# Performance work log

Measured on AMD Instinct MI355X. Metric: run time of the kernel, lower is better.

The kernel has to match this reference:

```python
import jax, jax.numpy as jnp
import numpy as np

B, S, F = 8, 8192, 11
D_MODEL, D_STATE, D_CONV, EXPAND, N_LAYERS = 128, 16, 4, 2, 4
D_INNER = EXPAND * D_MODEL
DT_RANK = (D_MODEL + 15) // 16  # ceil(d_model/16) = 8


def setup_inputs() -> dict:
    key = jax.random.key(0)
    ks = jax.random.split(key, 12)
    inp = {
        "features": jax.random.normal(ks[0], (B, S, F), jnp.float32),
        "emb_w": jax.random.normal(ks[1], (F, D_MODEL), jnp.float32) * 0.1,
        "emb_b": jnp.zeros((D_MODEL,), jnp.float32),
        "in_proj_w": jax.random.normal(ks[2], (N_LAYERS, D_MODEL, 2 * D_INNER), jnp.float32) * (D_MODEL ** -0.5),
        "conv_w": jax.random.normal(ks[3], (N_LAYERS, D_INNER, D_CONV), jnp.float32) * 0.3,
        "conv_b": jnp.zeros((N_LAYERS, D_INNER), jnp.float32),
        "x_proj_w": jax.random.normal(ks[4], (N_LAYERS, D_INNER, DT_RANK + 2 * D_STATE), jnp.float32) * (D_INNER ** -0.5),
        "dt_w": jax.random.normal(ks[5], (N_LAYERS, DT_RANK, D_INNER), jnp.float32) * (DT_RANK ** -0.5),
        "dt_b": jax.random.normal(ks[6], (N_LAYERS, D_INNER), jnp.float32) * 0.1 - 4.0,  # softplus -> small dt
        # canonical S4D-real init: A_log = log(1..d_state), per channel
        "A_log": jnp.broadcast_to(jnp.log(jnp.arange(1, D_STATE + 1, dtype=jnp.float32)), (N_LAYERS, D_INNER, D_STATE)).copy(),
        "D": jnp.ones((N_LAYERS, D_INNER), jnp.float32),
        "out_proj_w": jax.random.normal(ks[7], (N_LAYERS, D_INNER, D_MODEL), jnp.float32) * (D_INNER ** -0.5),
        "head_w": jax.random.normal(ks[8], (D_MODEL, 1), jnp.float32) * (D_MODEL ** -0.5),
        "head_b": jnp.zeros((1,), jnp.float32),
    }
    return inp


def _mamba_layer(x, in_w, cw, cb, xp_w, dtw, dtb, A_log, Dp, out_w):
    # x: [B,S,d_model]
    xz = x @ in_w                       # [B,S,2*d_inner]
    u, z = jnp.split(xz, 2, axis=-1)    # each [B,S,d_inner]
    # causal depthwise conv1d over sequence
    uc = jnp.transpose(u, (0, 2, 1))    # [B,d_inner,S]
    kern = cw[:, None, :]               # [d_inner,1,d_conv]
    conv = jax.lax.conv_general_dilated(
        uc, kern, window_strides=(1,), padding=[(D_CONV - 1, 0)],
        dimension_numbers=("NCH", "OIH", "NCH"), feature_group_count=D_INNER)
    u = jax.nn.silu(jnp.transpose(conv, (0, 2, 1)) + cb)   # [B,S,d_inner]
    x_dbl = u @ xp_w                                        # [B,S,dt_rank+2N]
    dt, Bm, Cm = jnp.split(x_dbl, [DT_RANK, DT_RANK + D_STATE], axis=-1)
    delta = jax.nn.softplus(dt @ dtw + dtb)                 # [B,S,d_inner]
    A = -jnp.exp(A_log)                                     # [d_inner,N]

    def step(h, inp):
        d_t, b_t, c_t, u_t = inp        # [B,d_inner],[B,N],[B,N],[B,d_inner]
        dA = jnp.exp(d_t[:, :, None] * A)                   # [B,d_inner,N]
        h = h * dA + (d_t * u_t)[:, :, None] * b_t[:, None, :]
        y = jnp.einsum("bdn,bn->bd", h, c_t)
        return h, y

    h0 = jnp.zeros((x.shape[0], D_INNER, D_STATE), x.dtype)
    xs = (jnp.transpose(delta, (1, 0, 2)), jnp.transpose(Bm, (1, 0, 2)),
          jnp.transpose(Cm, (1, 0, 2)), jnp.transpose(u, (1, 0, 2)))
    _, ys = jax.lax.scan(step, h0, xs)                      # ys: [S,B,d_inner]
    y = jnp.transpose(ys, (1, 0, 2)) + u * Dp
    y = y * jax.nn.silu(z)
    return y @ out_w                                        # [B,S,d_model]


def reference(features, emb_w, emb_b, in_proj_w, conv_w, conv_b, x_proj_w,
              dt_w, dt_b, A_log, D, out_proj_w, head_w, head_b):
    x = features @ emb_w + emb_b
    for i in range(N_LAYERS):
        x = _mamba_layer(x, in_proj_w[i], conv_w[i], conv_b[i], x_proj_w[i],
                         dt_w[i], dt_b[i], A_log[i], D[i], out_proj_w[i])
    logits = x @ head_w + head_b
    return jax.nn.sigmoid(logits)       # [B,S,1]
```

## Files before the change

kernel.cpp:

```cpp
#include <hip/hip_runtime.h>

#define BB 8
#define SS 8192
#define FF 11
#define DM 128
#define DSTATE 16
#define DI 256
#define NL 4
#define DTR 8
#define TT (BB*SS)
#define NCHUNK 256
#define LCHUNK (SS/NCHUNK)

typedef __bf16 bf16x8 __attribute__((ext_vector_type(8)));
typedef float f32x4 __attribute__((ext_vector_type(4)));

__device__ __forceinline__ ushort f2bf(float f) {
    union { float f; unsigned u; } v; v.f = f;
    unsigned r = v.u + 0x7FFF + ((v.u >> 16) & 1);
    return (ushort)(r >> 16);
}
__device__ __forceinline__ float b2f(ushort h) {
    union { unsigned u; float f; } v; v.u = ((unsigned)h) << 16;
    return v.f;
}
__device__ __forceinline__ float rcpf(float x) { return __builtin_amdgcn_rcpf(x); }

__device__ __forceinline__ void dA_powers(float e1, float* dA) {
    float p2 = e1 * e1, p4 = p2 * p2, p8 = p4 * p4;
    dA[0] = e1;  dA[1] = p2;       dA[2] = p2 * e1;  dA[3] = p4;
    dA[4] = p4 * e1; dA[5] = p4 * p2; dA[6] = p4 * dA[2]; dA[7] = p8;
#pragma unroll
    for (int i = 8; i < 16; ++i) dA[i] = p8 * dA[i - 8];
}

__device__ __forceinline__ void del_e1(float x, float& del, float& e1) {
    float ex = __expf(x);
    e1 = rcpf(1.f + ex);
    del = (x > 20.f) ? x : -__logf(e1);
}

__global__ void k_prep(const float* __restrict__ inpw, const float* __restrict__ xpw,
                       const float* __restrict__ outw, const float* __restrict__ ew,
                       const float* __restrict__ eb, const float* __restrict__ hw,
                       ushort* __restrict__ WtIn, ushort* __restrict__ WtXp,
                       ushort* __restrict__ WtOut, float* __restrict__ W1,
                       float* __restrict__ wh) {
    int task = blockIdx.y;
    int idx = blockIdx.x * 256 + threadIdx.x;
    if (task < 4) {
        int l = task, tot = 512 * 128;
        if (idx >= tot) return;
        int n = idx >> 7, k = idx & 127;
        float v = inpw[(size_t)l * 128 * 512 + (size_t)k * 512 + n];
        WtIn[(size_t)l * tot + idx] = f2bf(v);
    } else if (task < 8) {
        int l = task - 4, tot = 64 * 256;
        if (idx >= tot) return;
        int n = idx >> 8, k = idx & 255;
        float v = (n < 40) ? xpw[(size_t)l * 256 * 40 + (size_t)k * 40 + n] : 0.f;
        WtXp[(size_t)l * tot + idx] = f2bf(v);
    } else if (task < 12) {
        int l = task - 8, tot = 128 * 256;
        if (idx >= tot) return;
        int n = idx >> 8, k = idx & 255;
        float v = outw[(size_t)l * 256 * 128 + (size_t)k * 128 + n];
        WtOut[(size_t)l * tot + idx] = f2bf(v);
    } else if (task == 12) {
        if (idx >= 12 * 512) return;
        int f = idx >> 9, n = idx & 511;
        const float* src = (f < FF) ? (ew + f * DM) : eb;
        float acc = 0.f;
#pragma unroll 4
        for (int dm = 0; dm < DM; ++dm) acc = fmaf(src[dm], inpw[(size_t)dm * 512 + n], acc);
        W1[idx] = acc;
    } else {
        if (idx >= 256) return;
        float acc = 0.f;
#pragma unroll 4
        for (int dm = 0; dm < DM; ++dm)
            acc = fmaf(outw[(size_t)3 * DI * DM + (size_t)idx * DM + dm], hw[dm], acc);
        wh[idx] = acc;
    }
}

__global__ __launch_bounds__(256) void k_xz0(const float* __restrict__ feat,
                                             const float* __restrict__ W1,
                                             ushort* __restrict__ xz) {
    int tid = threadIdx.x;
    int n0 = (tid & 127) * 4;
    int rsub = tid >> 7;
    int r0 = blockIdx.x * 16 + rsub * 8;
    f32x4 wv[12];
#pragma unroll
    for (int f = 0; f < 12; ++f) wv[f] = *(const f32x4*)&W1[f * 512 + n0];
#pragma unroll
    for (int k = 0; k < 8; ++k) {
        int r = r0 + k;
        const float* fr = feat + (size_t)r * FF;
        f32x4 a = wv[11];
#pragma unroll
        for (int f = 0; f < FF; ++f) a += fr[f] * wv[f];
        ushort4 o;
        o.x = f2bf(a[0]); o.y = f2bf(a[1]); o.z = f2bf(a[2]); o.w = f2bf(a[3]);
        *(ushort4*)&xz[(size_t)r * 512 + n0] = o;
    }
}

template<bool OUT_BF16>
__global__ __launch_bounds__(256) void k_mgemm(const ushort* __restrict__ A,
                                               const ushort* __restrict__ Wt,
                                               void* __restrict__ Cv,
                                               int N, int K) {
    __shared__ __align__(16) ushort As[128 * 64];
    const int tid  = threadIdx.x;
    const int lane = tid & 63, wv = tid >> 6;
    const int m0 = blockIdx.x * 128;
    const int n0 = blockIdx.y * 64;
    const int lrow = lane >> 3;
    const int kcg  = (lane & 7) ^ lrow;
    const int mrow = lane & 15;
    const int kq   = lane >> 4;

    f32x4 acc[2][4];
#pragma unroll
    for (int i = 0; i < 2; ++i)
#pragma unroll
        for (int j = 0; j < 4; ++j) acc[i][j] = (f32x4){0.f, 0.f, 0.f, 0.f};

    const int rl0 = (wv << 5) + mrow;
    const int rl1 = rl0 + 16;
    const ushort* bg[4];
#pragma unroll
    for (int jt = 0; jt < 4; ++jt)
        bg[jt] = Wt + (size_t)(n0 + (jt << 4) + mrow) * K + (kq << 3);

    for (int k0 = 0; k0 < K; k0 += 64) {
        if (k0) __syncthreads();
#pragma unroll
        for (int i = 0; i < 4; ++i) {
            int issue = (wv << 2) + i;
            int row = (issue << 3) + lrow;
            const ushort* gp = A + (size_t)(m0 + row) * K + k0 + (kcg << 3);
            __builtin_amdgcn_global_load_lds(
                (const __attribute__((address_space(1))) void*)gp,
                (__attribute__((address_space(3))) void*)(As + (issue << 9)),
                16, 0, 0);
        }
        __syncthreads();
#pragma unroll
        for (int ks = 0; ks < 2; ++ks) {
            int kqg = (ks << 2) + kq;
            bf16x8 a0 = *(const bf16x8*)&As[(rl0 << 6) + ((kqg ^ (rl0 & 7)) << 3)];
            bf16x8 a1 = *(const bf16x8*)&As[(rl1 << 6) + ((kqg ^ (rl1 & 7)) << 3)];
#pragma unroll
            for (int jt = 0; jt < 4; ++jt) {
                bf16x8 b = *(const bf16x8*)(bg[jt] + k0 + (ks << 5));
                acc[0][jt] = __builtin_amdgcn_mfma_f32_16x16x32_bf16(a0, b, acc[0][jt], 0, 0, 0);
                acc[1][jt] = __builtin_amdgcn_mfma_f32_16x16x32_bf16(a1, b, acc[1][jt], 0, 0, 0);
            }
        }
    }
    int crow = m0 + (wv << 5) + (kq << 2);
    int ccol = n0 + mrow;
#pragma unroll
    for (int i = 0; i < 2; ++i)
#pragma unroll
        for (int jt = 0; jt < 4; ++jt)
#pragma unroll
            for (int rg = 0; rg < 4; ++rg) {
                int row = crow + (i << 4) + rg;
                int col = ccol + (jt << 4);
                if (OUT_BF16) {
                    ((ushort*)Cv)[(size_t)row * N + col] = f2bf(acc[i][jt][rg]);
                } else {
                    if (col < N) ((float*)Cv)[(size_t)row * N + col] = acc[i][jt][rg];
                }
            }
}

__global__ __launch_bounds__(256) void k_convxp(const ushort* __restrict__ xz,
                                                const float* __restrict__ cw,
                                                const float* __restrict__ cb,
                                                const ushort* __restrict__ WtXp_l,
                                                ushort* __restrict__ uc,
                                                float* __restrict__ xdbl) {
    __shared__ __align__(16) ushort us[32 * 256];
    int tid = threadIdx.x;
    int cg = tid & 63;
    int tsub = tid >> 6;
    int r0b = blockIdx.x * 32;
    int r0 = r0b + tsub * 8;
    int d0 = cg * 4;
    int tloc = r0 & (SS - 1);

    float w[4][4], bias[4];
#pragma unroll
    for (int j = 0; j < 4; ++j) {
        bias[j] = cb[d0 + j];
        float4 wj = *(const float4*)&cw[(d0 + j) * 4];
        w[j][0] = wj.x; w[j][1] = wj.y; w[j][2] = wj.z; w[j][3] = wj.w;
    }
    float xv[11][4];
#pragma unroll
    for (int i = 0; i < 11; ++i) {
        ushort4 v = make_ushort4(0, 0, 0, 0);
        if (tloc + i >= 3)
            v = *(const ushort4*)&xz[(size_t)(r0 + i - 3) * 512 + d0];
        xv[i][0] = b2f(v.x); xv[i][1] = b2f(v.y);
        xv[i][2] = b2f(v.z); xv[i][3] = b2f(v.w);
    }
#pragma unroll
    for (int k = 0; k < 8; ++k) {
        float a[4] = {bias[0], bias[1], bias[2], bias[3]};
#pragma unroll
        for (int j = 0; j < 4; ++j)
#pragma unroll
            for (int ch = 0; ch < 4; ++ch)
                a[ch] = fmaf(xv[k + j][ch], w[ch][j], a[ch]);
        ushort4 o;
        o.x = f2bf(a[0] * rcpf(1.f + __expf(-a[0])));
        o.y = f2bf(a[1] * rcpf(1.f + __expf(-a[1])));
        o.z = f2bf(a[2] * rcpf(1.f + __expf(-a[2])));
        o.w = f2bf(a[3] * rcpf(1.f + __expf(-a[3])));
        *(ushort4*)&uc[(size_t)(r0 + k) * DI + d0] = o;
        int lr = tsub * 8 + k;
        int addr = lr * 256 + (((cg >> 1) ^ (lr & 7)) << 3) + ((cg & 1) << 2);
        *(ushort4*)&us[addr] = o;
    }
    __syncthreads();
    int lane = tid & 63, wvi = tid >> 6;
    int mt = wvi & 1;
    int nt0 = (wvi >> 1) * 2;
    int mrow = lane & 15, kq = lane >> 4;
    f32x4 acc0 = (f32x4){0.f, 0.f, 0.f, 0.f};
    f32x4 acc1 = (f32x4){0.f, 0.f, 0.f, 0.f};
    int arow = mt * 16 + mrow;
    const ushort* bg0 = WtXp_l + (size_t)(nt0 * 16 + mrow) * 256 + (kq << 3);
    const ushort* bg1 = bg0 + 16 * 256;
#pragma unroll
    for (int k0 = 0; k0 < 256; k0 += 32) {
        int chunk = (k0 >> 3) + kq;
        bf16x8 a = *(const bf16x8*)&us[arow * 256 + ((chunk ^ (arow & 7)) << 3)];
        bf16x8 b0 = *(const bf16x8*)(bg0 + k0);
        bf16x8 b1 = *(const bf16x8*)(bg1 + k0);
        acc0 = __builtin_amdgcn_mfma_f32_16x16x32_bf16(a, b0, acc0, 0, 0, 0);
        acc1 = __builtin_amdgcn_mfma_f32_16x16x32_bf16(a, b1, acc1, 0, 0, 0);
    }
    int row = r0b + mt * 16 + (kq << 2);
    int col0 = nt0 * 16 + mrow;
    int col1 = col0 + 16;
#pragma unroll
    for (int rg = 0; rg < 4; ++rg) {
        if (col0 < 40) xdbl[(size_t)(row + rg) * 40 + col0] = acc0[rg];
        if (col1 < 40) xdbl[(size_t)(row + rg) * 40 + col1] = acc1[rg];
    }
}

__global__ __launch_bounds__(256) void k_scanA(const float* __restrict__ xdbl,
                                               ushort* __restrict__ uc,
                                               const float* __restrict__ dtw,
                                               const float* __restrict__ dtb,
                                               const float* __restrict__ Dp,
                                               ushort* __restrict__ hloc,
                                               float* __restrict__ sumd) {
    int d = threadIdx.x;
    int c = blockIdx.x & (NCHUNK - 1);
    int b = blockIdx.x >> 8;
    float wdt[8];
#pragma unroll
    for (int j = 0; j < 8; ++j) wdt[j] = dtw[j * DI + d];
    float bdt = dtb[d];
    float Dd = Dp[d];
    float h[16] = {};
    float sd = 0.f;
    size_t rbase = (size_t)(b * SS + c * LCHUNK);
    const float* __restrict__ rwp = xdbl + rbase * 40;
    ushort* __restrict__ up = uc + rbase * DI + d;
    float ut = b2f(up[0]);
    float cur[40];
#pragma unroll
    for (int j = 0; j < 40; ++j) cur[j] = rwp[j];
    for (int tt = 0; tt < LCHUNK; ++tt) {
        float nxt[40];
        const float* rn = rwp + (tt + 1) * 40;
#pragma unroll
        for (int j = 0; j < 40; ++j) nxt[j] = rn[j];
        float utn = b2f(up[(tt + 1) * DI]);
        float x = bdt;
#pragma unroll
        for (int j = 0; j < 8; ++j) x = fmaf(cur[j], wdt[j], x);
        float del, e1;
        del_e1(x, del, e1);
        float du = del * ut;
        float dA[16];
        dA_powers(e1, dA);
        float y = 0.f;
#pragma unroll
        for (int n = 0; n < 16; ++n) {
            h[n] = fmaf(h[n], dA[n], du * cur[8 + n]);
            y = fmaf(h[n], cur[24 + n], y);
        }
        sd += del;
        up[tt * DI] = f2bf(fmaf(ut, Dd, y));
        ut = utn;
#pragma unroll
        for (int j = 0; j < 40; ++j) cur[j] = nxt[j];
    }
    size_t o = (size_t)(b * NCHUNK + c) * DI + d;
    sumd[o] = sd;
    uint4 s0, s1;
    s0.x = (unsigned)f2bf(h[0])  | ((unsigned)f2bf(h[1])  << 16);
    s0.y = (unsigned)f2bf(h[2])  | ((unsigned)f2bf(h[3])  << 16);
    s0.z = (unsigned)f2bf(h[4])  | ((unsigned)f2bf(h[5])  << 16);
    s0.w = (unsigned)f2bf(h[6])  | ((unsigned)f2bf(h[7])  << 16);
    s1.x = (unsigned)f2bf(h[8])  | ((unsigned)f2bf(h[9])  << 16);
    s1.y = (unsigned)f2bf(h[10]) | ((unsigned)f2bf(h[11]) << 16);
    s1.z = (unsigned)f2bf(h[12]) | ((unsigned)f2bf(h[13]) << 16);
    s1.w = (unsigned)f2bf(h[14]) | ((unsigned)f2bf(h[15]) << 16);
    *(uint4*)&hloc[o * 16] = s0;
    *(uint4*)&hloc[o * 16 + 8] = s1;
}

__global__ void k_scanB(const ushort* __restrict__ hloc, const float* __restrict__ sumd,
                        const float* __restrict__ Alog, ushort* __restrict__ hinit) {
    int idx = blockIdx.x * 256 + threadIdx.x;
    int n = idx & 15;
    int d = (idx >> 4) & 255;
    int b = idx >> 12;
    float Av = -__expf(Alog[d * 16 + n]);
    float H = 0.f;
    size_t base = (size_t)(b * NCHUNK) * DI + d;
    float sd8[8], hl8[8];
#pragma unroll
    for (int k = 0; k < 8; ++k) {
        size_t o = base + (size_t)k * DI;
        sd8[k] = sumd[o];
        hl8[k] = b2f(hloc[o * 16 + n]);
    }
    for (int c = 0; c < NCHUNK; c += 8) {
        float nsd[8], nhl[8];
        if (c + 8 < NCHUNK) {
#pragma unroll
            for (int k = 0; k < 8; ++k) {
                size_t o = base + (size_t)(c + 8 + k) * DI;
                nsd[k] = sumd[o];
                nhl[k] = b2f(hloc[o * 16 + n]);
            }
        }
#pragma unroll
        for (int k = 0; k < 8; ++k) {
            size_t o = base + (size_t)(c + k) * DI;
            hinit[o * 16 + n] = f2bf(H);
            H = fmaf(H, __expf(Av * sd8[k]), hl8[k]);
        }
#pragma unroll
        for (int k = 0; k < 8; ++k) { sd8[k] = nsd[k]; hl8[k] = nhl[k]; }
    }
}

template<bool DO_HEAD>
__global__ __launch_bounds__(256) void k_scanC2(const float* __restrict__ xdbl,
                                                ushort* __restrict__ uc,
                                                const ushort* __restrict__ xz,
                                                const float* __restrict__ dtw,
                                                const float* __restrict__ dtb,
                                                const ushort* __restrict__ hinit,
                                                const float* __restrict__ wh,
                                                const float* __restrict__ hb,
                                                float* __restrict__ outp) {
    int d = threadIdx.x;
    int c = blockIdx.x & (NCHUNK - 1);
    int b = blockIdx.x >> 8;
    float wdt[8];
#pragma unroll
    for (int j = 0; j < 8; ++j) wdt[j] = dtw[j * DI + d];
    float bdt = dtb[d];
    float whd = DO_HEAD ? wh[d] : 0.f;
    __shared__ float hpart[LCHUNK][4];
    int lane = threadIdx.x & 63, wv4 = threadIdx.x >> 6;
    float g[16];
    size_t oh = ((size_t)(b * NCHUNK + c) * DI + d) * 16;
    {
        uint4 s0 = *(const uint4*)&hinit[oh];
        uint4 s1 = *(const uint4*)&hinit[oh + 8];
        g[0]  = b2f((ushort)(s0.x & 0xffff)); g[1]  = b2f((ushort)(s0.x >> 16));
        g[2]  = b2f((ushort)(s0.y & 0xffff)); g[3]  = b2f((ushort)(s0.y >> 16));
        g[4]  = b2f((ushort)(s0.z & 0xffff)); g[5]  = b2f((ushort)(s0.z >> 16));
        g[6]  = b2f((ushort)(s0.w & 0xffff)); g[7]  = b2f((ushort)(s0.w >> 16));
        g[8]  = b2f((ushort)(s1.x & 0xffff)); g[9]  = b2f((ushort)(s1.x >> 16));
        g[10] = b2f((ushort)(s1.y & 0xffff)); g[11] = b2f((ushort)(s1.y >> 16));
        g[12] = b2f((ushort)(s1.z & 0xffff)); g[13] = b2f((ushort)(s1.z >> 16));
        g[14] = b2f((ushort)(s1.w & 0xffff)); g[15] = b2f((ushort)(s1.w >> 16));
    }
    size_t rbase = (size_t)(b * SS + c * LCHUNK);
    const float* __restrict__ rwp = xdbl + rbase * 40;
    ushort* __restrict__ up = uc + rbase * DI + d;
    const ushort* __restrict__ zp = xz + rbase * 512 + 256 + d;
    float E = 1.f;
    float cur[24];
#pragma unroll
    for (int j = 0; j < 8; ++j) cur[j] = rwp[j];
#pragma unroll
    for (int j = 0; j < 16; ++j) cur[8 + j] = rwp[24 + j];
    for (int tt = 0; tt < LCHUNK; ++tt) {
        float nxt[24];
        const float* rn = rwp + (tt + 1) * 40;
#pragma unroll
        for (int j = 0; j < 8; ++j) nxt[j] = rn[j];
#pragma unroll
        for (int j = 0; j < 16; ++j) nxt[8 + j] = rn[24 + j];
        float zt = b2f(zp[tt * 512]);
        float yp = b2f(up[tt * DI]);
        float x = bdt;
#pragma unroll
        for (int j = 0; j < 8; ++j) x = fmaf(cur[j], wdt[j], x);
        float e1 = rcpf(1.f + __expf(x));
        E *= e1;
        float dA[16];
        dA_powers(E, dA);
        float corr = 0.f;
#pragma unroll
        for (int n = 0; n < 16; ++n)
            corr = fmaf(dA[n] * g[n], cur[8 + n], corr);
        float y = yp + corr;
        float yo = y * (zt * rcpf(1.f + __expf(-zt)));
        if (DO_HEAD) {
            float p = yo * whd;
#pragma unroll
            for (int off = 32; off; off >>= 1) p += __shfl_xor(p, off, 64);
            if (lane == 0) hpart[tt][wv4] = p;
        } else {
            up[tt * DI] = f2bf(yo);
        }
#pragma unroll
        for (int j = 0; j < 24; ++j) cur[j] = nxt[j];
    }
    if (DO_HEAD) {
        __syncthreads();
        if (threadIdx.x < LCHUNK) {
            float s = hpart[threadIdx.x][0] + hpart[threadIdx.x][1] +
                      hpart[threadIdx.x][2] + hpart[threadIdx.x][3];
            outp[rbase + threadIdx.x] = 1.f / (1.f + __expf(-(s + hb[0])));
        }
    }
}

extern "C" void kernel_launch(void* const* d_in, const int* in_sizes, int n_in,
                              void* d_out, int out_size, void* d_ws, size_t ws_size,
                              hipStream_t stream) {
    const float* feat   = (const float*)d_in[0];
    const float* emb_w  = (const float*)d_in[1];
    const float* emb_b  = (const float*)d_in[2];
    const float* inpw   = (const float*)d_in[3];
    const float* convw  = (const float*)d_in[4];
    const float* convb  = (const float*)d_in[5];
    const float* xpw    = (const float*)d_in[6];
    const float* dtw    = (const float*)d_in[7];
    const float* dtb    = (const float*)d_in[8];
    const float* alog   = (const float*)d_in[9];
    const float* Dp     = (const float*)d_in[10];
    const float* outw   = (const float*)d_in[11];
    const float* headw  = (const float*)d_in[12];
    const float* headb  = (const float*)d_in[13];
    float* outp = (float*)d_out;

    char* w = (char*)d_ws;
    ushort* WtIn  = (ushort*)w;  w += (size_t)NL * 512 * 128 * 2;
    ushort* WtXp  = (ushort*)w;  w += (size_t)NL * 64 * 256 * 2;
    ushort* WtOut = (ushort*)w;  w += (size_t)NL * 128 * 256 * 2;
    float*  W1    = (float*)w;   w += (size_t)12 * 512 * 4;
    float*  whf   = (float*)w;   w += (size_t)256 * 4;
    ushort* xbuf  = (ushort*)w;  w += (size_t)TT * 128 * 2;
    ushort* xz    = (ushort*)w;  w += (size_t)TT * 512 * 2;
    ushort* ucb   = (ushort*)w;  w += (size_t)TT * 256 * 2;
    float*  xdbl  = (float*)w;   w += (size_t)TT * 40 * 4;
    ushort* hloc  = (ushort*)w;  w += (size_t)NCHUNK * BB * DI * 16 * 2;
    float*  sumd  = (float*)w;   w += (size_t)NCHUNK * BB * DI * 4;
    ushort* hinit = (ushort*)w;

    k_prep<<<dim3(256, 14), 256, 0, stream>>>(inpw, xpw, outw, emb_w, emb_b, headw,
                                              WtIn, WtXp, WtOut, W1, whf);

    for (int l = 0; l < NL; ++l) {
        const float* cw_l   = convw + (size_t)l * DI * 4;
        const float* cb_l   = convb + (size_t)l * DI;
        const float* dtw_l  = dtw   + (size_t)l * DTR * DI;
        const float* dtb_l  = dtb   + (size_t)l * DI;
        const float* alog_l = alog  + (size_t)l * DI * DSTATE;
        const float* Dp_l   = Dp    + (size_t)l * DI;

        if (l == 0)
            k_xz0<<<TT / 16, 256, 0, stream>>>(feat, W1, xz);
        else
            k_mgemm<true><<<dim3(TT / 128, 8), 256, 0, stream>>>(xbuf, WtIn + (size_t)l * 512 * 128, xz, 512, 128);
        k_convxp<<<TT / 32, 256, 0, stream>>>(xz, cw_l, cb_l, WtXp + (size_t)l * 64 * 256, ucb, xdbl);
        k_scanA<<<BB * NCHUNK, 256, 0, stream>>>(xdbl, ucb, dtw_l, dtb_l, Dp_l, hloc, sumd);
        k_scanB<<<BB * DI * 16 / 256, 256, 0, stream>>>(hloc, sumd, alog_l, hinit);
        if (l < NL - 1) {
            k_scanC2<false><<<BB * NCHUNK, 256, 0, stream>>>(xdbl, ucb, xz, dtw_l, dtb_l, hinit,
                                                             whf, headb, outp);
            k_mgemm<true><<<dim3(TT / 128, 2), 256, 0, stream>>>(ucb, WtOut + (size_t)l * 128 * 256, xbuf, 128, 256);
        } else {
            k_scanC2<true><<<BB * NCHUNK, 256, 0, stream>>>(xdbl, ucb, xz, dtw_l, dtb_l, hinit,
                                                            whf, headb, outp);
        }
    }
}
```

Measured before the change: 848.8 us.

## Fuse out_proj GEMM into scan output kernel via shared-memory tile

The scan output kernel now keeps its 32x256 gated y tile in XOR-swizzled shared memory instead of writing it to global. After a block barrier it runs a 32x128 bf16 MFMA GEMM against the layer's out_proj weights and writes the next layer's input directly. This removes a separate GEMM launch and the global round trip of the y activations. In exchange it adds 16KB of LDS per block, which may lower occupancy, and each block re-reads the full 128x256 weight matrix from global/L2.

```diff
diff --git a/kernel.cpp b/kernel.cpp
--- a/kernel.cpp
+++ b/kernel.cpp
@@ -366,9 +366,13 @@
                                                 const float* __restrict__ dtw,
                                                 const float* __restrict__ dtb,
                                                 const ushort* __restrict__ hinit,
+                                                const ushort* __restrict__ WtOut_l,
+                                                ushort* __restrict__ xbuf,
                                                 const float* __restrict__ wh,
                                                 const float* __restrict__ hb,
                                                 float* __restrict__ outp) {
+    __shared__ __align__(16) ushort us[32 * 256];
+    float* hpart = (float*)us;
     int d = threadIdx.x;
     int c = blockIdx.x & (NCHUNK - 1);
     int b = blockIdx.x >> 8;
@@ -377,7 +381,6 @@
     for (int j = 0; j < 8; ++j) wdt[j] = dtw[j * DI + d];
     float bdt = dtb[d];
     float whd = DO_HEAD ? wh[d] : 0.f;
-    __shared__ float hpart[LCHUNK][4];
     int lane = threadIdx.x & 63, wv4 = threadIdx.x >> 6;
     float g[16];
     size_t oh = ((size_t)(b * NCHUNK + c) * DI + d) * 16;
@@ -429,19 +432,51 @@
             float p = yo * whd;
 #pragma unroll
             for (int off = 32; off; off >>= 1) p += __shfl_xor(p, off, 64);
-            if (lane == 0) hpart[tt][wv4] = p;
+            if (lane == 0) hpart[tt * 4 + wv4] = p;
         } else {
-            up[tt * DI] = f2bf(yo);
+            int addr = tt * 256 + (((d >> 3) ^ (tt & 7)) << 3) + (d & 7);
+            us[addr] = f2bf(yo);
         }
 #pragma unroll
         for (int j = 0; j < 24; ++j) cur[j] = nxt[j];
     }
+    __syncthreads();
     if (DO_HEAD) {
-        __syncthreads();
         if (threadIdx.x < LCHUNK) {
-            float s = hpart[threadIdx.x][0] + hpart[threadIdx.x][1] +
-                      hpart[threadIdx.x][2] + hpart[threadIdx.x][3];
+            float s = hpart[threadIdx.x * 4 + 0] + hpart[threadIdx.x * 4 + 1] +
+                      hpart[threadIdx.x * 4 + 2] + hpart[threadIdx.x * 4 + 3];
             outp[rbase + threadIdx.x] = 1.f / (1.f + __expf(-(s + hb[0])));
+        }
+    } else {
+        int wvi = threadIdx.x >> 6;
+        int mt = wvi & 1;
+        int ntbase = (wvi >> 1) * 4;
+        int mrow = lane & 15, kq = lane >> 4;
+        int arow = mt * 16 + mrow;
+        f32x4 acc[4];
+#pragma unroll
+        for (int j = 0; j < 4; ++j) acc[j] = (f32x4){0.f, 0.f, 0.f, 0.f};
+        const ushort* bg[4];
+#pragma unroll
+        for (int j = 0; j < 4; ++j)
+            bg[j] = WtOut_l + (size_t)((ntbase + j) * 16 + mrow) * 256 + (kq << 3);
+#pragma unroll
+        for (int k0 = 0; k0 < 256; k0 += 32) {
+            int chunk = (k0 >> 3) + kq;
+            bf16x8 a = *(const bf16x8*)&us[arow * 256 + ((chunk ^ (arow & 7)) << 3)];
+#pragma unroll
+            for (int j = 0; j < 4; ++j) {
+                bf16x8 bfr = *(const bf16x8*)(bg[j] + k0);
+                acc[j] = __builtin_amdgcn_mfma_f32_16x16x32_bf16(a, bfr, acc[j], 0, 0, 0);
+            }
+        }
+        int row = mt * 16 + (kq << 2);
+#pragma unroll
+        for (int j = 0; j < 4; ++j) {
+            int col = (ntbase + j) * 16 + mrow;
+#pragma unroll
+            for (int rg = 0; rg < 4; ++rg)
+                xbuf[(rbase + row + rg) * DM + col] = f2bf(acc[j][rg]);
         }
     }
 }
@@ -497,13 +532,12 @@
         k_convxp<<<TT / 32, 256, 0, stream>>>(xz, cw_l, cb_l, WtXp + (size_t)l * 64 * 256, ucb, xdbl);
         k_scanA<<<BB * NCHUNK, 256, 0, stream>>>(xdbl, ucb, dtw_l, dtb_l, Dp_l, hloc, sumd);
         k_scanB<<<BB * DI * 16 / 256, 256, 0, stream>>>(hloc, sumd, alog_l, hinit);
-        if (l < NL - 1) {
+        if (l < NL - 1)
             k_scanC2<false><<<BB * NCHUNK, 256, 0, stream>>>(xdbl, ucb, xz, dtw_l, dtb_l, hinit,
+                                                             WtOut + (size_t)l * 128 * 256, xbuf,
                                                              whf, headb, outp);
-            k_mgemm<true><<<dim3(TT / 128, 2), 256, 0, stream>>>(ucb, WtOut + (size_t)l * 128 * 256, xbuf, 128, 256);
-        } else {
+        else
             k_scanC2<true><<<BB * NCHUNK, 256, 0, stream>>>(xdbl, ucb, xz, dtw_l, dtb_l, hinit,
-                                                            whf, headb, outp);
-        }
-    }
-}
+                                                            WtOut, xbuf, whf, headb, outp);
+    }
+}
```

New measurement: 832.8 us. No clear change (-1.9%).
